# Kernel optimization log

Hardware: AMD Instinct MI355X
Metric: run time of the kernel (lower is better)

## Reference

```python
import jax, jax.numpy as jnp
import numpy as np

NUM_FEATURES = 128
NUM_FILTERS = 128

def setup_inputs() -> dict:
    key = jax.random.key(0)
    k1, k2, k3, k4, k5 = jax.random.split(key, 5)
    B, N, F = 4, 2048, NUM_FEATURES
    x = jax.random.normal(k1, (B, N, F), dtype=jnp.float32)
    A = jax.random.normal(k2, (B, N, N), dtype=jnp.float32)
    # Conv1D(num_filters, kernel_size=1, use_bias=False) == per-node linear F -> filters
    W = jax.random.normal(k3, (F, NUM_FILTERS), dtype=jnp.float32) * (1.0 / np.sqrt(F))
    # self.a: Conv1D(1, kernel_size=1) with bias == linear filters -> 1 (shared for x_i and x_j)
    a_w = jax.random.normal(k4, (NUM_FILTERS, 1), dtype=jnp.float32) * (1.0 / np.sqrt(NUM_FILTERS))
    a_b = jax.random.normal(k5, (1,), dtype=jnp.float32) * 0.01
    bias = jnp.zeros((NUM_FILTERS,), dtype=jnp.float32)
    return {"x": x, "A": A, "W": W, "a_w": a_w, "a_b": a_b, "bias": bias}

def reference(x, A, W, a_w, a_b, bias):
    # project features: [B,N,F] @ [F,Ff] -> [B,N,Ff]
    h = jnp.einsum('bnf,fg->bng', x, W)
    # shared attention projection (x_i and x_j use the same layer): [B,N,1]
    s = jnp.einsum('bng,go->bno', h, a_w) + a_b
    # additive scores s_i + s_j^T -> [B,N,N]
    e = s + jnp.swapaxes(s, 1, 2)
    e = jnp.where(e >= 0, e, 0.2 * e)  # LeakyReLU(0.2)
    attn = jax.nn.softmax(e + A, axis=-1)
    out = jnp.einsum('bij,bjg->big', attn, h) + bias
    return out
```

## Files before the change

### kernel.cpp

```cpp
#include <hip/hip_runtime.h>
#include <hip/hip_bf16.h>
#include <stdint.h>

#define BB 4
#define NN 2048
#define FF 128

typedef __attribute__((ext_vector_type(8))) short bf16x8;
typedef __attribute__((ext_vector_type(4))) float f32x4;

__device__ inline unsigned pk_bf16(float a, float b) {
    union { float f; unsigned u; } x, y;
    x.f = a; y.f = b;
    unsigned xu = x.u + (0x7fffu + ((x.u >> 16) & 1u));
    unsigned yu = y.u + (0x7fffu + ((y.u >> 16) & 1u));
    return (xu >> 16) | (yu & 0xffff0000u);
}

#define XT_P 136
#define WT_P 136

__global__ __launch_bounds__(256) void k1_proj(
    const float* __restrict__ x, const float* __restrict__ W,
    const float* __restrict__ a_w, const float* __restrict__ a_b,
    uint16_t* __restrict__ Ht, float* __restrict__ s_out)
{
    __shared__ uint16_t xt[16 * XT_P];
    __shared__ uint16_t Wt[128 * WT_P];
    __shared__ float sredw[4 * 16];

    const int t = threadIdx.x;
    const int w = t >> 6, l = t & 63;
    const int m16 = l & 15, q = l >> 4;
    const int b = blockIdx.x >> 7;
    const int n0 = (blockIdx.x & 127) << 4;

    const int c4 = (t & 31) * 4, kh = (t >> 5) * 16;
    float4 wr0[8], wr1[8];
    #pragma unroll
    for (int kk = 0; kk < 8; ++kk) {
        const int k = kh + 2 * kk;
        wr0[kk] = *(const float4*)(W + (size_t)k * 128 + c4);
        wr1[kk] = *(const float4*)(W + (size_t)(k + 1) * 128 + c4);
    }
    {
        const int row = t >> 4, c0 = (t & 15) * 8;
        const float* xr = x + ((size_t)(b * NN + n0 + row)) * FF + c0;
        const float4 v0 = *(const float4*)xr;
        const float4 v1 = *(const float4*)(xr + 4);
        unsigned* dst = (unsigned*)(xt + row * XT_P + c0);
        dst[0] = pk_bf16(v0.x, v0.y); dst[1] = pk_bf16(v0.z, v0.w);
        dst[2] = pk_bf16(v1.x, v1.y); dst[3] = pk_bf16(v1.z, v1.w);
    }
    #pragma unroll
    for (int kk = 0; kk < 8; ++kk) {
        const int k = kh + 2 * kk;
        *(unsigned*)(Wt + (c4 + 0) * WT_P + k) = pk_bf16(wr0[kk].x, wr1[kk].x);
        *(unsigned*)(Wt + (c4 + 1) * WT_P + k) = pk_bf16(wr0[kk].y, wr1[kk].y);
        *(unsigned*)(Wt + (c4 + 2) * WT_P + k) = pk_bf16(wr0[kk].z, wr1[kk].z);
        *(unsigned*)(Wt + (c4 + 3) * WT_P + k) = pk_bf16(wr0[kk].w, wr1[kk].w);
    }
    const int g0 = (2 * w) * 16 + m16, g1 = (2 * w + 1) * 16 + m16;
    const float aw0 = a_w[g0], aw1 = a_w[g1];
    __syncthreads();

    f32x4 acc0 = {}, acc1 = {};
    bf16x8 af[4];
    #pragma unroll
    for (int dk = 0; dk < 4; ++dk)
        af[dk] = *(const bf16x8*)(xt + m16 * XT_P + dk * 32 + q * 8);
    #pragma unroll
    for (int dk = 0; dk < 4; ++dk) {
        bf16x8 b0 = *(const bf16x8*)(Wt + g0 * WT_P + dk * 32 + q * 8);
        bf16x8 b1 = *(const bf16x8*)(Wt + g1 * WT_P + dk * 32 + q * 8);
        acc0 = __builtin_amdgcn_mfma_f32_16x16x32_bf16(af[dk], b0, acc0, 0, 0, 0);
        acc1 = __builtin_amdgcn_mfma_f32_16x16x32_bf16(af[dk], b1, acc1, 0, 0, 0);
    }

    float sp[4];
    #pragma unroll
    for (int r = 0; r < 4; ++r) sp[r] = acc0[r] * aw0 + acc1[r] * aw1;
    #pragma unroll
    for (int off = 1; off < 16; off <<= 1)
        #pragma unroll
        for (int r = 0; r < 4; ++r) sp[r] += __shfl_xor(sp[r], off, 64);
    if (m16 == 0) {
        #pragma unroll
        for (int r = 0; r < 4; ++r) sredw[w * 16 + q * 4 + r] = sp[r];
    }
    {
        uint2 o0 = { pk_bf16(acc0[0], acc0[1]), pk_bf16(acc0[2], acc0[3]) };
        uint2 o1 = { pk_bf16(acc1[0], acc1[1]), pk_bf16(acc1[2], acc1[3]) };
        *(uint2*)(Ht + ((size_t)(b * 128 + g0)) * NN + n0 + q * 4) = o0;
        *(uint2*)(Ht + ((size_t)(b * 128 + g1)) * NN + n0 + q * 4) = o1;
    }
    __syncthreads();
    if (t < 16)
        s_out[b * NN + n0 + t] = sredw[t] + sredw[16 + t] + sredw[32 + t] + sredw[48 + t] + a_b[0];
}

#define JS 8
#define IRND 8

__global__ __launch_bounds__(256, 2) void k2_attn(
    const float* __restrict__ A, const uint16_t* __restrict__ Ht,
    const float* __restrict__ s, uint16_t* __restrict__ po,
    float* __restrict__ prs)
{
    __shared__ float Opw[4][16 * 132];
    __shared__ float rsw[4][16];

    const int t = threadIdx.x;
    const int w = t >> 6, l = t & 63;
    const int m16 = l & 15, q = l >> 4;

    const int bx = blockIdx.x;
    const int js = bx & 7;
    const int is = (bx >> 3) & 15;
    const int b  = bx >> 7;
    const int j0 = js * 256;
    const int ibase = is * 128;

    const float* sb = s + b * NN;
    const float* Ab = A + (size_t)b * NN * NN;
    const uint16_t* Hb = Ht + (size_t)b * FF * NN;

    const int jc0 = j0 + w * 32 + q * 8;
    const int jc1 = j0 + (w + 4) * 32 + q * 8;

    float4 sj00 = *(const float4*)(sb + jc0);
    float4 sj01 = *(const float4*)(sb + jc0 + 4);
    float4 sj10 = *(const float4*)(sb + jc1);
    float4 sj11 = *(const float4*)(sb + jc1 + 4);

    bf16x8 hf0[8], hf1[8];
    #pragma unroll
    for (int gt = 0; gt < 8; ++gt) {
        const uint16_t* hp = Hb + (size_t)(gt * 16 + m16) * NN;
        hf0[gt] = *(const bf16x8*)(hp + jc0);
        hf1[gt] = *(const bf16x8*)(hp + jc1);
    }

    const float* Ar = Ab + (size_t)(ibase + m16) * NN;
    float4 a00 = *(const float4*)(Ar + jc0);
    float4 a01 = *(const float4*)(Ar + jc0 + 4);
    float4 a10 = *(const float4*)(Ar + jc1);
    float4 a11 = *(const float4*)(Ar + jc1 + 4);
    float si = sb[ibase + m16];

    const size_t slice = (size_t)(js * BB + b);

    for (int r = 0; r < IRND; ++r) {
        const int i0r = ibase + r * 16;
        const int i0n = ibase + ((r + 1) & (IRND - 1)) * 16;

        const float* An = Ab + (size_t)(i0n + m16) * NN;
        float4 n00 = *(const float4*)(An + jc0);
        float4 n01 = *(const float4*)(An + jc0 + 4);
        float4 n10 = *(const float4*)(An + jc1);
        float4 n11 = *(const float4*)(An + jc1 + 4);
        const float sin_ = sb[i0n + m16];

        const float svv[16] = {sj00.x,sj00.y,sj00.z,sj00.w, sj01.x,sj01.y,sj01.z,sj01.w,
                               sj10.x,sj10.y,sj10.z,sj10.w, sj11.x,sj11.y,sj11.z,sj11.w};
        const float avv[16] = {a00.x,a00.y,a00.z,a00.w, a01.x,a01.y,a01.z,a01.w,
                               a10.x,a10.y,a10.z,a10.w, a11.x,a11.y,a11.z,a11.w};
        float pv[16]; float rs = 0.f;
        #pragma unroll
        for (int j = 0; j < 16; ++j) {
            float e = si + svv[j];
            e = fmaxf(e, 0.2f * e);
            pv[j] = __expf(e + avv[j]);
            rs += pv[j];
        }
        union { unsigned u[4]; bf16x8 v; } fa0, fa1;
        #pragma unroll
        for (int j = 0; j < 4; ++j) {
            fa0.u[j] = pk_bf16(pv[2 * j], pv[2 * j + 1]);
            fa1.u[j] = pk_bf16(pv[8 + 2 * j], pv[9 + 2 * j]);
        }

        f32x4 acc[8];
        #pragma unroll
        for (int gt = 0; gt < 8; ++gt) {
            f32x4 z = {0.f, 0.f, 0.f, 0.f};
            z = __builtin_amdgcn_mfma_f32_16x16x32_bf16(fa0.v, hf0[gt], z, 0, 0, 0);
            acc[gt] = __builtin_amdgcn_mfma_f32_16x16x32_bf16(fa1.v, hf1[gt], z, 0, 0, 0);
        }

        rs += __shfl_xor(rs, 16, 64);
        rs += __shfl_xor(rs, 32, 64);
        if (q == 0) rsw[w][m16] = rs;

        #pragma unroll
        for (int gt = 0; gt < 8; ++gt)
            #pragma unroll
            for (int rr = 0; rr < 4; ++rr)
                Opw[w][(q * 4 + rr) * 132 + gt * 16 + m16] = acc[gt][rr];
        asm volatile("s_waitcnt lgkmcnt(0)\n\ts_barrier" ::: "memory");

        {
            const int row = t >> 4, k8 = (t & 15) * 8;
            float v[8] = {0.f,0.f,0.f,0.f,0.f,0.f,0.f,0.f};
            #pragma unroll
            for (int sl = 0; sl < 4; ++sl) {
                float4 u0 = *(const float4*)&Opw[sl][row * 132 + k8];
                float4 u1 = *(const float4*)&Opw[sl][row * 132 + k8 + 4];
                v[0] += u0.x; v[1] += u0.y; v[2] += u0.z; v[3] += u0.w;
                v[4] += u1.x; v[5] += u1.y; v[6] += u1.z; v[7] += u1.w;
            }
            unsigned* op = (unsigned*)(po + ((slice * NN + i0r + row) * FF + k8));
            op[0] = pk_bf16(v[0], v[1]); op[1] = pk_bf16(v[2], v[3]);
            op[2] = pk_bf16(v[4], v[5]); op[3] = pk_bf16(v[6], v[7]);
            if (t < 16)
                prs[slice * NN + i0r + t] = rsw[0][t] + rsw[1][t] + rsw[2][t] + rsw[3][t];
        }
        asm volatile("s_waitcnt lgkmcnt(0)\n\ts_barrier" ::: "memory");

        a00 = n00; a01 = n01; a10 = n10; a11 = n11; si = sin_;
    }
}

__global__ __launch_bounds__(256) void k3_red(
    const uint16_t* __restrict__ po, const float* __restrict__ prs,
    const float* __restrict__ bias, float* __restrict__ out)
{
    const int idx = blockIdx.x * 256 + threadIdx.x;
    const int g = idx & 127;
    const int i = (idx >> 7) & (NN - 1);
    const int b = idx >> 18;
    float sum = 0.f, rsum = 0.f;
    #pragma unroll
    for (int js = 0; js < JS; ++js) {
        const size_t base = (size_t)(js * BB + b) * NN + i;
        union { unsigned u; float f; } cv;
        cv.u = ((unsigned)po[base * FF + g]) << 16;
        sum += cv.f;
        rsum += prs[base];
    }
    out[idx] = sum / rsum + bias[g];
}

extern "C" void kernel_launch(void* const* d_in, const int* in_sizes, int n_in,
                              void* d_out, int out_size, void* d_ws, size_t ws_size,
                              hipStream_t stream) {
    const float* x    = (const float*)d_in[0];
    const float* A    = (const float*)d_in[1];
    const float* W    = (const float*)d_in[2];
    const float* a_w  = (const float*)d_in[3];
    const float* a_b  = (const float*)d_in[4];
    const float* bias = (const float*)d_in[5];
    float* out = (float*)d_out;

    char* ws = (char*)d_ws;
    uint16_t* Ht = (uint16_t*)ws;
    float* s = (float*)(ws + 2 * 1024 * 1024);
    uint16_t* po = (uint16_t*)(ws + 2 * 1024 * 1024 + 65536);
    float* prs = (float*)(ws + 2 * 1024 * 1024 + 65536 + (size_t)JS * BB * NN * FF * 2);

    k1_proj<<<BB * (NN / 16), 256, 0, stream>>>(x, W, a_w, a_b, Ht, s);
    k2_attn<<<JS * 16 * BB, 256, 0, stream>>>(A, Ht, s, po, prs);
    k3_red<<<(BB * NN * FF) / 256, 256, 0, stream>>>(po, prs, bias, out);
}
```

Before: 124.9 us.

## Split attention work across 8 waves by feature half and vectorize reduction

The attention kernel moves from 4 waves to 8 waves per block. Each wave now covers half of the 128 output features and a 64-column slice of j, so it holds half as many H fragments in registers. The launch bound allows 3 blocks per CU, giving more waves in flight to hide the latency of the A and H loads. The cost is that the exponent and row-sum work and the A loads are duplicated across each feature-half wave pair. The final reduction kernel now processes 4 features per thread with vector loads and stores, and multiplies by a reciprocal instead of dividing.

New measurement: 128.5 us. 1.03x slower.

```diff
diff --git a/kernel.cpp b/kernel.cpp
--- a/kernel.cpp
+++ b/kernel.cpp
@@ -102,17 +102,18 @@
 #define JS 8
 #define IRND 8
 
-__global__ __launch_bounds__(256, 2) void k2_attn(
+__global__ __launch_bounds__(512, 3) void k2_attn(
     const float* __restrict__ A, const uint16_t* __restrict__ Ht,
     const float* __restrict__ s, uint16_t* __restrict__ po,
     float* __restrict__ prs)
 {
-    __shared__ float Opw[4][16 * 132];
+    __shared__ float Opw[8][16 * 68];
     __shared__ float rsw[4][16];
 
     const int t = threadIdx.x;
     const int w = t >> 6, l = t & 63;
     const int m16 = l & 15, q = l >> 4;
+    const int gh = w & 1, jh = w >> 1;
 
     const int bx = blockIdx.x;
     const int js = bx & 7;
@@ -125,27 +126,28 @@
     const float* Ab = A + (size_t)b * NN * NN;
     const uint16_t* Hb = Ht + (size_t)b * FF * NN;
 
-    const int jc0 = j0 + w * 32 + q * 8;
-    const int jc1 = j0 + (w + 4) * 32 + q * 8;
-
-    float4 sj00 = *(const float4*)(sb + jc0);
-    float4 sj01 = *(const float4*)(sb + jc0 + 4);
-    float4 sj10 = *(const float4*)(sb + jc1);
-    float4 sj11 = *(const float4*)(sb + jc1 + 4);
-
-    bf16x8 hf0[8], hf1[8];
-    #pragma unroll
-    for (int gt = 0; gt < 8; ++gt) {
-        const uint16_t* hp = Hb + (size_t)(gt * 16 + m16) * NN;
-        hf0[gt] = *(const bf16x8*)(hp + jc0);
-        hf1[gt] = *(const bf16x8*)(hp + jc1);
+    const int jcb = j0 + jh * 64;
+    const int jq0 = jcb + q * 8;
+    const int jq1 = jcb + 32 + q * 8;
+
+    float4 sj0 = *(const float4*)(sb + jq0);
+    float4 sj1 = *(const float4*)(sb + jq0 + 4);
+    float4 sj2 = *(const float4*)(sb + jq1);
+    float4 sj3 = *(const float4*)(sb + jq1 + 4);
+
+    bf16x8 hf[4][2];
+    #pragma unroll
+    for (int gt = 0; gt < 4; ++gt) {
+        const uint16_t* hp = Hb + (size_t)(gh * 64 + gt * 16 + m16) * NN;
+        hf[gt][0] = *(const bf16x8*)(hp + jq0);
+        hf[gt][1] = *(const bf16x8*)(hp + jq1);
     }
 
     const float* Ar = Ab + (size_t)(ibase + m16) * NN;
-    float4 a00 = *(const float4*)(Ar + jc0);
-    float4 a01 = *(const float4*)(Ar + jc0 + 4);
-    float4 a10 = *(const float4*)(Ar + jc1);
-    float4 a11 = *(const float4*)(Ar + jc1 + 4);
+    float4 a0 = *(const float4*)(Ar + jq0);
+    float4 a1 = *(const float4*)(Ar + jq0 + 4);
+    float4 a2 = *(const float4*)(Ar + jq1);
+    float4 a3 = *(const float4*)(Ar + jq1 + 4);
     float si = sb[ibase + m16];
 
     const size_t slice = (size_t)(js * BB + b);
@@ -155,16 +157,16 @@
         const int i0n = ibase + ((r + 1) & (IRND - 1)) * 16;
 
         const float* An = Ab + (size_t)(i0n + m16) * NN;
-        float4 n00 = *(const float4*)(An + jc0);
-        float4 n01 = *(const float4*)(An + jc0 + 4);
-        float4 n10 = *(const float4*)(An + jc1);
-        float4 n11 = *(const float4*)(An + jc1 + 4);
+        float4 n0 = *(const float4*)(An + jq0);
+        float4 n1 = *(const float4*)(An + jq0 + 4);
+        float4 n2 = *(const float4*)(An + jq1);
+        float4 n3 = *(const float4*)(An + jq1 + 4);
         const float sin_ = sb[i0n + m16];
 
-        const float svv[16] = {sj00.x,sj00.y,sj00.z,sj00.w, sj01.x,sj01.y,sj01.z,sj01.w,
-                               sj10.x,sj10.y,sj10.z,sj10.w, sj11.x,sj11.y,sj11.z,sj11.w};
-        const float avv[16] = {a00.x,a00.y,a00.z,a00.w, a01.x,a01.y,a01.z,a01.w,
-                               a10.x,a10.y,a10.z,a10.w, a11.x,a11.y,a11.z,a11.w};
+        const float svv[16] = {sj0.x,sj0.y,sj0.z,sj0.w, sj1.x,sj1.y,sj1.z,sj1.w,
+                               sj2.x,sj2.y,sj2.z,sj2.w, sj3.x,sj3.y,sj3.z,sj3.w};
+        const float avv[16] = {a0.x,a0.y,a0.z,a0.w, a1.x,a1.y,a1.z,a1.w,
+                               a2.x,a2.y,a2.z,a2.w, a3.x,a3.y,a3.z,a3.w};
         float pv[16]; float rs = 0.f;
         #pragma unroll
         for (int j = 0; j < 16; ++j) {
@@ -180,44 +182,45 @@
             fa1.u[j] = pk_bf16(pv[8 + 2 * j], pv[9 + 2 * j]);
         }
 
-        f32x4 acc[8];
-        #pragma unroll
-        for (int gt = 0; gt < 8; ++gt) {
+        f32x4 acc[4];
+        #pragma unroll
+        for (int gt = 0; gt < 4; ++gt) {
             f32x4 z = {0.f, 0.f, 0.f, 0.f};
-            z = __builtin_amdgcn_mfma_f32_16x16x32_bf16(fa0.v, hf0[gt], z, 0, 0, 0);
-            acc[gt] = __builtin_amdgcn_mfma_f32_16x16x32_bf16(fa1.v, hf1[gt], z, 0, 0, 0);
+            z = __builtin_amdgcn_mfma_f32_16x16x32_bf16(fa0.v, hf[gt][0], z, 0, 0, 0);
+            acc[gt] = __builtin_amdgcn_mfma_f32_16x16x32_bf16(fa1.v, hf[gt][1], z, 0, 0, 0);
         }
 
         rs += __shfl_xor(rs, 16, 64);
         rs += __shfl_xor(rs, 32, 64);
-        if (q == 0) rsw[w][m16] = rs;
-
-        #pragma unroll
-        for (int gt = 0; gt < 8; ++gt)
+        if (gh == 0 && q == 0) rsw[jh][m16] = rs;
+
+        #pragma unroll
+        for (int gt = 0; gt < 4; ++gt)
             #pragma unroll
             for (int rr = 0; rr < 4; ++rr)
-                Opw[w][(q * 4 + rr) * 132 + gt * 16 + m16] = acc[gt][rr];
+                Opw[w][(q * 4 + rr) * 68 + gt * 16 + m16] = acc[gt][rr];
         asm volatile("s_waitcnt lgkmcnt(0)\n\ts_barrier" ::: "memory");
 
         {
-            const int row = t >> 4, k8 = (t & 15) * 8;
-            float v[8] = {0.f,0.f,0.f,0.f,0.f,0.f,0.f,0.f};
+            const int row = t >> 5;
+            const int c4 = (t & 31) * 4;
+            const int gh2 = c4 >> 6;
+            const int cc = c4 & 63;
+            float4 v = {0.f, 0.f, 0.f, 0.f};
             #pragma unroll
-            for (int sl = 0; sl < 4; ++sl) {
-                float4 u0 = *(const float4*)&Opw[sl][row * 132 + k8];
-                float4 u1 = *(const float4*)&Opw[sl][row * 132 + k8 + 4];
-                v[0] += u0.x; v[1] += u0.y; v[2] += u0.z; v[3] += u0.w;
-                v[4] += u1.x; v[5] += u1.y; v[6] += u1.z; v[7] += u1.w;
+            for (int jh2 = 0; jh2 < 4; ++jh2) {
+                float4 u = *(const float4*)&Opw[jh2 * 2 + gh2][row * 68 + cc];
+                v.x += u.x; v.y += u.y; v.z += u.z; v.w += u.w;
             }
-            unsigned* op = (unsigned*)(po + ((slice * NN + i0r + row) * FF + k8));
-            op[0] = pk_bf16(v[0], v[1]); op[1] = pk_bf16(v[2], v[3]);
-            op[2] = pk_bf16(v[4], v[5]); op[3] = pk_bf16(v[6], v[7]);
+            unsigned* op = (unsigned*)(po + ((slice * NN + i0r + row) * FF + c4));
+            op[0] = pk_bf16(v.x, v.y);
+            op[1] = pk_bf16(v.z, v.w);
             if (t < 16)
                 prs[slice * NN + i0r + t] = rsw[0][t] + rsw[1][t] + rsw[2][t] + rsw[3][t];
         }
         asm volatile("s_waitcnt lgkmcnt(0)\n\ts_barrier" ::: "memory");
 
-        a00 = n00; a01 = n01; a10 = n10; a11 = n11; si = sin_;
+        a0 = n0; a1 = n1; a2 = n2; a3 = n3; si = sin_;
     }
 }
 
@@ -226,19 +229,25 @@
     const float* __restrict__ bias, float* __restrict__ out)
 {
     const int idx = blockIdx.x * 256 + threadIdx.x;
-    const int g = idx & 127;
-    const int i = (idx >> 7) & (NN - 1);
-    const int b = idx >> 18;
-    float sum = 0.f, rsum = 0.f;
+    const int g4 = (idx & 31) * 4;
+    const int i = (idx >> 5) & (NN - 1);
+    const int b = idx >> 16;
+
+    float v0 = 0.f, v1 = 0.f, v2 = 0.f, v3 = 0.f, rsum = 0.f;
     #pragma unroll
     for (int js = 0; js < JS; ++js) {
         const size_t base = (size_t)(js * BB + b) * NN + i;
-        union { unsigned u; float f; } cv;
-        cv.u = ((unsigned)po[base * FF + g]) << 16;
-        sum += cv.f;
+        uint2 u = *(const uint2*)(po + base * FF + g4);
+        union { unsigned u; float f; } c0, c1, c2, c3;
+        c0.u = u.x << 16; c1.u = u.x & 0xffff0000u;
+        c2.u = u.y << 16; c3.u = u.y & 0xffff0000u;
+        v0 += c0.f; v1 += c1.f; v2 += c2.f; v3 += c3.f;
         rsum += prs[base];
     }
-    out[idx] = sum / rsum + bias[g];
+    const float inv = 1.0f / rsum;
+    float4 bv = *(const float4*)(bias + g4);
+    float4 o = { v0 * inv + bv.x, v1 * inv + bv.y, v2 * inv + bv.z, v3 * inv + bv.w };
+    *(float4*)(out + ((size_t)b * NN + i) * FF + g4) = o;
 }
 
 extern "C" void kernel_launch(void* const* d_in, const int* in_sizes, int n_in,
@@ -259,6 +268,6 @@
     float* prs = (float*)(ws + 2 * 1024 * 1024 + 65536 + (size_t)JS * BB * NN * FF * 2);
 
     k1_proj<<<BB * (NN / 16), 256, 0, stream>>>(x, W, a_w, a_b, Ht, s);
-    k2_attn<<<JS * 16 * BB, 256, 0, stream>>>(A, Ht, s, po, prs);
-    k3_red<<<(BB * NN * FF) / 256, 256, 0, stream>>>(po, prs, bias, out);
-}
+    k2_attn<<<JS * 16 * BB, 512, 0, stream>>>(A, Ht, s, po, prs);
+    k3_red<<<(BB * NN * 32) / 256, 256, 0, stream>>>(po, prs, bias, out);
+}
```
